# Performance work log

Measured on AMD Instinct MI355X. Metric: run time of the kernel, lower is better.

## Reference

```python
import jax, jax.numpy as jnp
import numpy as np

EPS_TRAP = 1e-8
EPS_F32 = float(np.finfo(np.float32).eps)


def _trapmf(x, a, b, c, d):
    # All args broadcastable; returns trapezoidal membership in [0,1].
    rise = (x - a) / (b - a + EPS_TRAP)
    fall = (d - x) / (d - c + EPS_TRAP)
    y = jnp.zeros_like(x + a)
    y = jnp.where((a < x) & (x < b), rise, y)
    y = jnp.where((b <= x) & (x <= c), 1.0, y)
    y = jnp.where((c < x) & (x < d), fall, y)
    return y


def setup_inputs() -> dict:
    key = jax.random.key(0)
    k1, k2, k3 = jax.random.split(key, 3)
    batch, in_dim, out_dim, n_rules = 4096, 64, 64, 256
    lo, hi = -1.0, 2.0
    x = jax.random.uniform(k1, (batch, in_dim), jnp.float32, lo, hi)
    # sorted per last-dim to satisfy a<=b<=c<=d (BreakpointIncreasingOrderConstraint)
    Antes = jnp.sort(jax.random.uniform(k2, (n_rules, in_dim, 4), jnp.float32, lo, hi), axis=-1)
    Cons = jnp.sort(jax.random.uniform(k3, (n_rules, out_dim, 4), jnp.float32, lo, hi), axis=-1)
    return {"x": x, "Antes": Antes, "Cons": Cons}


def reference(x, Antes, Cons):
    # x: (batch, in_dim); Antes: (n_rules, in_dim, 4); Cons: (n_rules, out_dim, 4)
    a = Antes[:, None, :, 0]  # (n_rules, 1, in_dim)
    b = Antes[:, None, :, 1]
    c = Antes[:, None, :, 2]
    d = Antes[:, None, :, 3]
    memb = _trapmf(x[None, :, :], a, b, c, d)      # (n_rules, batch, in_dim)
    w = jnp.min(memb, axis=-1).T                   # (batch, n_rules)
    w = w[:, :, None]                              # (batch, n_rules, 1)

    A = Cons[None, :, :, 0]  # (1, n_rules, out_dim)
    B = Cons[None, :, :, 1]
    C = Cons[None, :, :, 2]
    D = Cons[None, :, :, 3]

    term1 = 3.0 * w * (D**2 - A**2) * (1.0 - w)
    term2 = 3.0 * w**2 * (C * D - A * B)
    term3 = w**3 * (C - D + A - B) * (C - D - A + B)
    num = term1 + term2 + term3                    # (batch, n_rules, out_dim)
    den = 2.0 * w * (D - A) + w**2 * (C + A - D - B) + EPS_F32

    num_sum = num.sum(axis=1)                      # (batch, out_dim)
    den_sum = den.sum(axis=1)
    Ys = jnp.where(den_sum != 0, num_sum / den_sum, 0.0)
    return Ys / 3.0
```

## Files before the change

kernel.cpp:

```cpp
#include <hip/hip_runtime.h>


#define EPS_TRAP 1e-8f
#define EPS_F32  1.1920928955078125e-07f

constexpr int BATCH   = 4096;
constexpr int IN_DIM  = 64;
constexpr int OUT_DIM = 64;
constexpr int N_RULES = 256;

__global__ __launch_bounds__(256) void w_kernel(
    const float*  __restrict__ x,
    const float4* __restrict__ Antes,
    float* __restrict__ W,
    unsigned* __restrict__ flags)
{
    __shared__ float xs[IN_DIM][65];

    int tid  = threadIdx.x;
    int nblk = blockIdx.x & 63;
    int rgrp = blockIdx.x >> 6;
    int n0   = nblk * 64;

    #pragma unroll
    for (int k = 0; k < 4; ++k) {
        int flat = tid + k * 256;
        int nl = flat >> 4;
        int i4 = (flat & 15) * 4;
        float4 v = *reinterpret_cast<const float4*>(x + (n0 + nl) * IN_DIM + i4);
        xs[i4 + 0][nl] = v.x;
        xs[i4 + 1][nl] = v.y;
        xs[i4 + 2][nl] = v.z;
        xs[i4 + 3][nl] = v.w;
    }
    __syncthreads();

    int lane = tid & 63;
    int wvu  = __builtin_amdgcn_readfirstlane(tid >> 6);
    int r0   = rgrp * 64 + wvu * 16;

    unsigned mask = 0;
    for (int g = 0; g < 4; ++g) {
        int rb4 = r0 + g * 4;
        const float4* __restrict__ ap = Antes + rb4 * IN_DIM;

        float m[4] = {1e30f, 1e30f, 1e30f, 1e30f};
        for (int ib = 0; ib < IN_DIM; ib += 8) {
            #pragma unroll
            for (int io = 0; io < 8; ++io) {
                int i = ib + io;
                float xv = xs[i][lane];
                #pragma unroll
                for (int rr = 0; rr < 4; ++rr) {
                    float4 q = ap[rr * IN_DIM + i];
                    m[rr] = fminf(m[rr], fminf(xv - q.x, q.w - xv));
                }
            }
            float mx = fmaxf(fmaxf(m[0], m[1]), fmaxf(m[2], m[3]));
            if (!__any(mx > 0.0f)) break;
        }

        unsigned gf = 0;
        #pragma unroll
        for (int rr = 0; rr < 4; ++rr)
            if (__any(m[rr] > 0.0f)) gf |= 1u << rr;

        if (gf) {
            for (int rr = 0; rr < 4; ++rr) {
                if (!(gf & (1u << rr))) continue;
                const float4* __restrict__ aq = ap + rr * IN_DIM;
                float wm = 1e30f;
                for (int i = 0; i < IN_DIM; ++i) {
                    float4 q = aq[i];
                    float iba = 1.0f / (q.y - q.x + EPS_TRAP);
                    float idc = 1.0f / (q.w - q.z + EPS_TRAP);
                    float xv = xs[i][lane];
                    wm = fminf(wm, fminf((xv - q.x) * iba, (q.w - xv) * idc));
                }
                float w = fminf(fmaxf(wm, 0.0f), 1.0f);
                W[(rb4 + rr) * BATCH + n0 + lane] = w;
            }
        }
        mask |= gf << (g * 4);
    }
    if (lane == 0) flags[nblk * 16 + rgrp * 4 + wvu] = mask;
}

__global__ __launch_bounds__(256) void combine_kernel(
    const float*  __restrict__ W,
    const float4* __restrict__ Cons,
    const unsigned* __restrict__ flags,
    float* __restrict__ out)
{
    __shared__ unsigned fw[16];
    __shared__ float lN[4][16][64];
    __shared__ float lD[4][16][64];

    int tid   = threadIdx.x;
    int nbase = blockIdx.x * 16;
    int nblk  = blockIdx.x >> 2;

    if (tid < 16) fw[tid] = flags[nblk * 16 + tid];
    __syncthreads();

    unsigned any = 0;
    #pragma unroll
    for (int i = 0; i < 16; ++i) any |= fw[i];

    if (any == 0u) {
        reinterpret_cast<float4*>(out)[blockIdx.x * 256 + tid] =
            make_float4(0.f, 0.f, 0.f, 0.f);
        return;
    }

    int lane = tid & 63;
    int wv   = __builtin_amdgcn_readfirstlane(tid >> 6);

    unsigned long long mask =
        (unsigned long long)fw[wv * 4 + 0]        |
        ((unsigned long long)fw[wv * 4 + 1] << 16) |
        ((unsigned long long)fw[wv * 4 + 2] << 32) |
        ((unsigned long long)fw[wv * 4 + 3] << 48);
    int rbase = wv * 64;

    float num[16], den[16];
    #pragma unroll
    for (int k = 0; k < 16; ++k) { num[k] = 0.0f; den[k] = 0.0f; }

    while (mask) {
        int lr = __ffsll(mask) - 1;
        mask &= mask - 1;
        int r = rbase + lr;

        float4 c = Cons[r * OUT_DIM + lane];
        float A = c.x, B = c.y, C = c.z, D = c.w;
        float c1 = 3.0f * (D * D - A * A);
        float c2 = 3.0f * (C * D - A * B) - c1;
        float c3 = (C - D + A - B) * (C - D - A + B);
        float d1 = 2.0f * (D - A);
        float d2 = C + A - D - B;

        const float* __restrict__ wp = W + r * BATCH + nbase;
        #pragma unroll
        for (int k = 0; k < 16; ++k) {
            float w = wp[k];
            float tn = fmaf(fmaf(c3, w, c2), w, c1);
            num[k] = fmaf(tn, w, num[k]);
            den[k] = fmaf(fmaf(d2, w, d1), w, den[k]);
        }
    }

    #pragma unroll
    for (int k = 0; k < 16; ++k) { lN[wv][k][lane] = num[k]; lD[wv][k][lane] = den[k]; }
    __syncthreads();

    #pragma unroll
    for (int kk = 0; kk < 4; ++kk) {
        int row = (tid >> 6) * 4 + kk;
        float n = lN[0][row][lane] + lN[1][row][lane] +
                  lN[2][row][lane] + lN[3][row][lane];
        float d = lD[0][row][lane] + lD[1][row][lane] +
                  lD[2][row][lane] + lD[3][row][lane];
        d += (float)N_RULES * EPS_F32;
        out[(nbase + row) * OUT_DIM + lane] = (d != 0.0f) ? (n / d) * (1.0f / 3.0f) : 0.0f;
    }
}

__global__ __launch_bounds__(256) void fused_kernel(
    const float*  __restrict__ x,
    const float4* __restrict__ Antes,
    const float4* __restrict__ Cons,
    float* __restrict__ out)
{
    __shared__ float xs[IN_DIM][9];
    __shared__ float wl[N_RULES][9];

    int n0 = blockIdx.x * 8;
    int t  = threadIdx.x;

    for (int k = 0; k < 2; ++k) {
        int idx = t * 2 + k;
        int nl = idx >> 6, i = idx & 63;
        xs[i][nl] = x[(n0 + nl) * IN_DIM + i];
    }
    __syncthreads();

    {
        float wmin[8];
        #pragma unroll
        for (int n = 0; n < 8; ++n) wmin[n] = 1e30f;
        const float4* ap = Antes + t * IN_DIM;
        for (int i = 0; i < IN_DIM; ++i) {
            float4 q = ap[i];
            float iba = 1.0f / (q.y - q.x + EPS_TRAP);
            float idc = 1.0f / (q.w - q.z + EPS_TRAP);
            float na = -q.x * iba, dq = q.w * idc;
            #pragma unroll
            for (int n = 0; n < 8; ++n) {
                float xv = xs[i][n];
                float y = fminf(fmaf(xv, iba, na), fmaf(xv, -idc, dq));
                y = fminf(fmaxf(y, 0.0f), 1.0f);
                wmin[n] = fminf(wmin[n], y);
            }
        }
        #pragma unroll
        for (int n = 0; n < 8; ++n) wl[t][n] = wmin[n];
    }
    __syncthreads();

    int lane = t & 63, wv = t >> 6;
    float num0 = 0.f, den0 = 0.f, num1 = 0.f, den1 = 0.f;
    for (int r = 0; r < N_RULES; ++r) {
        float4 c = Cons[r * OUT_DIM + lane];
        float A = c.x, B = c.y, C = c.z, D = c.w;
        float c1 = 3.0f * (D * D - A * A);
        float c2 = 3.0f * (C * D - A * B) - c1;
        float c3 = (C - D + A - B) * (C - D - A + B);
        float d1 = 2.0f * (D - A);
        float d2 = C + A - D - B;
        float wa = wl[r][wv * 2], wb = wl[r][wv * 2 + 1];
        float wa2 = wa * wa, wa3 = wa2 * wa;
        float wb2 = wb * wb, wb3 = wb2 * wb;
        num0 = fmaf(c1, wa, num0); num0 = fmaf(c2, wa2, num0); num0 = fmaf(c3, wa3, num0);
        den0 = fmaf(d1, wa, den0); den0 = fmaf(d2, wa2, den0);
        num1 = fmaf(c1, wb, num1); num1 = fmaf(c2, wb2, num1); num1 = fmaf(c3, wb3, num1);
        den1 = fmaf(d1, wb, den1); den1 = fmaf(d2, wb2, den1);
    }
    den0 += 256.0f * EPS_F32;
    den1 += 256.0f * EPS_F32;
    float y0 = (den0 != 0.0f) ? num0 / den0 : 0.0f;
    float y1 = (den1 != 0.0f) ? num1 / den1 : 0.0f;
    out[(n0 + wv * 2) * OUT_DIM + lane]     = y0 * (1.0f / 3.0f);
    out[(n0 + wv * 2 + 1) * OUT_DIM + lane] = y1 * (1.0f / 3.0f);
}

extern "C" void kernel_launch(void* const* d_in, const int* in_sizes, int n_in,
                              void* d_out, int out_size, void* d_ws, size_t ws_size,
                              hipStream_t stream) {
    const float* x     = (const float*)d_in[0];
    const float* Antes = (const float*)d_in[1];
    const float* Cons  = (const float*)d_in[2];
    float* out = (float*)d_out;

    const size_t W_BYTES  = (size_t)N_RULES * BATCH * 4;
    const size_t FL_BYTES = 64 * 16 * sizeof(unsigned);
    const size_t NEED = W_BYTES + FL_BYTES;

    if (ws_size >= NEED) {
        char* p = (char*)d_ws;
        float*    Wp    = (float*)p;      p += W_BYTES;
        unsigned* flags = (unsigned*)p;

        w_kernel<<<256, 256, 0, stream>>>(x, (const float4*)Antes, Wp, flags);
        combine_kernel<<<256, 256, 0, stream>>>(Wp, (const float4*)Cons, flags, out);
    } else {
        fused_kernel<<<512, 256, 0, stream>>>(x, (const float4*)Antes,
                                              (const float4*)Cons, out);
    }
}
```

Before: 14.90 us.

## Fuse membership and combine kernels into one block-per-64-rows kernel using LDS

Merges the two-kernel pipeline (a firing-strength kernel writing W and flags to global workspace, then a combine kernel) into one kernel with 1024-thread blocks. Each block handles 64 batch rows, keeps the rule weights and active-rule flags in shared memory, and then accumulates the consequent terms over only the active rules. This removes the second launch and the global round trip of the W matrix. In exchange the grid shrinks to 64 large blocks, which leaves many CUs idle, and the per-block work on the Antes scan grows.

```diff
diff --git a/kernel.cpp b/kernel.cpp
--- a/kernel.cpp
+++ b/kernel.cpp
@@ -9,24 +9,22 @@
 constexpr int OUT_DIM = 64;
 constexpr int N_RULES = 256;
 
-__global__ __launch_bounds__(256) void w_kernel(
+__global__ __launch_bounds__(1024) void fuzzy_fused_kernel(
     const float*  __restrict__ x,
     const float4* __restrict__ Antes,
-    float* __restrict__ W,
-    unsigned* __restrict__ flags)
+    const float4* __restrict__ Cons,
+    float* __restrict__ out)
 {
-    __shared__ float xs[IN_DIM][65];
+    __shared__ float    xs[IN_DIM][65];
+    __shared__ float    Wlds[N_RULES][64];
+    __shared__ unsigned fl[16];
 
-    int tid  = threadIdx.x;
-    int nblk = blockIdx.x & 63;
-    int rgrp = blockIdx.x >> 6;
-    int n0   = nblk * 64;
+    int tid = threadIdx.x;
+    int n0  = blockIdx.x * 64;
 
-    #pragma unroll
-    for (int k = 0; k < 4; ++k) {
-        int flat = tid + k * 256;
-        int nl = flat >> 4;
-        int i4 = (flat & 15) * 4;
+    {
+        int nl = tid >> 4;
+        int i4 = (tid & 15) * 4;
         float4 v = *reinterpret_cast<const float4*>(x + (n0 + nl) * IN_DIM + i4);
         xs[i4 + 0][nl] = v.x;
         xs[i4 + 1][nl] = v.y;
@@ -37,9 +35,9 @@
 
     int lane = tid & 63;
     int wvu  = __builtin_amdgcn_readfirstlane(tid >> 6);
-    int r0   = rgrp * 64 + wvu * 16;
+    int r0   = wvu * 16;
 
-    unsigned mask = 0;
+    unsigned bits = 0;
     for (int g = 0; g < 4; ++g) {
         int rb4 = r0 + g * 4;
         const float4* __restrict__ ap = Antes + rb4 * IN_DIM;
@@ -77,161 +75,66 @@
                     float xv = xs[i][lane];
                     wm = fminf(wm, fminf((xv - q.x) * iba, (q.w - xv) * idc));
                 }
-                float w = fminf(fmaxf(wm, 0.0f), 1.0f);
-                W[(rb4 + rr) * BATCH + n0 + lane] = w;
+                Wlds[rb4 + rr][lane] = fminf(fmaxf(wm, 0.0f), 1.0f);
             }
         }
-        mask |= gf << (g * 4);
+        bits |= gf << (g * 4);
     }
-    if (lane == 0) flags[nblk * 16 + rgrp * 4 + wvu] = mask;
-}
-
-__global__ __launch_bounds__(256) void combine_kernel(
-    const float*  __restrict__ W,
-    const float4* __restrict__ Cons,
-    const unsigned* __restrict__ flags,
-    float* __restrict__ out)
-{
-    __shared__ unsigned fw[16];
-    __shared__ float lN[4][16][64];
-    __shared__ float lD[4][16][64];
-
-    int tid   = threadIdx.x;
-    int nbase = blockIdx.x * 16;
-    int nblk  = blockIdx.x >> 2;
-
-    if (tid < 16) fw[tid] = flags[nblk * 16 + tid];
+    if (lane == 0) fl[wvu] = bits;
     __syncthreads();
 
     unsigned any = 0;
     #pragma unroll
-    for (int i = 0; i < 16; ++i) any |= fw[i];
+    for (int i = 0; i < 16; ++i) any |= fl[i];
 
     if (any == 0u) {
-        reinterpret_cast<float4*>(out)[blockIdx.x * 256 + tid] =
+        reinterpret_cast<float4*>(out)[blockIdx.x * 1024 + tid] =
             make_float4(0.f, 0.f, 0.f, 0.f);
         return;
     }
 
-    int lane = tid & 63;
-    int wv   = __builtin_amdgcn_readfirstlane(tid >> 6);
+    float num[4] = {0.f, 0.f, 0.f, 0.f};
+    float den[4] = {0.f, 0.f, 0.f, 0.f};
+    int row0 = wvu * 4;
 
-    unsigned long long mask =
-        (unsigned long long)fw[wv * 4 + 0]        |
-        ((unsigned long long)fw[wv * 4 + 1] << 16) |
-        ((unsigned long long)fw[wv * 4 + 2] << 32) |
-        ((unsigned long long)fw[wv * 4 + 3] << 48);
-    int rbase = wv * 64;
+    #pragma unroll
+    for (int w4 = 0; w4 < 4; ++w4) {
+        unsigned long long mask =
+            (unsigned long long)__builtin_amdgcn_readfirstlane(fl[w4 * 4 + 0])        |
+            ((unsigned long long)__builtin_amdgcn_readfirstlane(fl[w4 * 4 + 1]) << 16) |
+            ((unsigned long long)__builtin_amdgcn_readfirstlane(fl[w4 * 4 + 2]) << 32) |
+            ((unsigned long long)__builtin_amdgcn_readfirstlane(fl[w4 * 4 + 3]) << 48);
+        int rbase = w4 * 64;
 
-    float num[16], den[16];
-    #pragma unroll
-    for (int k = 0; k < 16; ++k) { num[k] = 0.0f; den[k] = 0.0f; }
+        while (mask) {
+            int lr = __ffsll(mask) - 1;
+            mask &= mask - 1;
+            int r = rbase + lr;
 
-    while (mask) {
-        int lr = __ffsll(mask) - 1;
-        mask &= mask - 1;
-        int r = rbase + lr;
+            float4 c = Cons[r * OUT_DIM + lane];
+            float A = c.x, B = c.y, C = c.z, D = c.w;
+            float c1 = 3.0f * (D * D - A * A);
+            float c2 = 3.0f * (C * D - A * B) - c1;
+            float c3 = (C - D + A - B) * (C - D - A + B);
+            float d1 = 2.0f * (D - A);
+            float d2 = C + A - D - B;
 
-        float4 c = Cons[r * OUT_DIM + lane];
-        float A = c.x, B = c.y, C = c.z, D = c.w;
-        float c1 = 3.0f * (D * D - A * A);
-        float c2 = 3.0f * (C * D - A * B) - c1;
-        float c3 = (C - D + A - B) * (C - D - A + B);
-        float d1 = 2.0f * (D - A);
-        float d2 = C + A - D - B;
-
-        const float* __restrict__ wp = W + r * BATCH + nbase;
-        #pragma unroll
-        for (int k = 0; k < 16; ++k) {
-            float w = wp[k];
-            float tn = fmaf(fmaf(c3, w, c2), w, c1);
-            num[k] = fmaf(tn, w, num[k]);
-            den[k] = fmaf(fmaf(d2, w, d1), w, den[k]);
+            #pragma unroll
+            for (int k = 0; k < 4; ++k) {
+                float w = Wlds[r][row0 + k];
+                float tn = fmaf(fmaf(c3, w, c2), w, c1);
+                num[k] = fmaf(tn, w, num[k]);
+                den[k] = fmaf(fmaf(d2, w, d1), w, den[k]);
+            }
         }
     }
 
     #pragma unroll
-    for (int k = 0; k < 16; ++k) { lN[wv][k][lane] = num[k]; lD[wv][k][lane] = den[k]; }
-    __syncthreads();
-
-    #pragma unroll
-    for (int kk = 0; kk < 4; ++kk) {
-        int row = (tid >> 6) * 4 + kk;
-        float n = lN[0][row][lane] + lN[1][row][lane] +
-                  lN[2][row][lane] + lN[3][row][lane];
-        float d = lD[0][row][lane] + lD[1][row][lane] +
-                  lD[2][row][lane] + lD[3][row][lane];
-        d += (float)N_RULES * EPS_F32;
-        out[(nbase + row) * OUT_DIM + lane] = (d != 0.0f) ? (n / d) * (1.0f / 3.0f) : 0.0f;
+    for (int k = 0; k < 4; ++k) {
+        float d = den[k] + (float)N_RULES * EPS_F32;
+        out[(n0 + row0 + k) * OUT_DIM + lane] =
+            (d != 0.0f) ? (num[k] / d) * (1.0f / 3.0f) : 0.0f;
     }
-}
-
-__global__ __launch_bounds__(256) void fused_kernel(
-    const float*  __restrict__ x,
-    const float4* __restrict__ Antes,
-    const float4* __restrict__ Cons,
-    float* __restrict__ out)
-{
-    __shared__ float xs[IN_DIM][9];
-    __shared__ float wl[N_RULES][9];
-
-    int n0 = blockIdx.x * 8;
-    int t  = threadIdx.x;
-
-    for (int k = 0; k < 2; ++k) {
-        int idx = t * 2 + k;
-        int nl = idx >> 6, i = idx & 63;
-        xs[i][nl] = x[(n0 + nl) * IN_DIM + i];
-    }
-    __syncthreads();
-
-    {
-        float wmin[8];
-        #pragma unroll
-        for (int n = 0; n < 8; ++n) wmin[n] = 1e30f;
-        const float4* ap = Antes + t * IN_DIM;
-        for (int i = 0; i < IN_DIM; ++i) {
-            float4 q = ap[i];
-            float iba = 1.0f / (q.y - q.x + EPS_TRAP);
-            float idc = 1.0f / (q.w - q.z + EPS_TRAP);
-            float na = -q.x * iba, dq = q.w * idc;
-            #pragma unroll
-            for (int n = 0; n < 8; ++n) {
-                float xv = xs[i][n];
-                float y = fminf(fmaf(xv, iba, na), fmaf(xv, -idc, dq));
-                y = fminf(fmaxf(y, 0.0f), 1.0f);
-                wmin[n] = fminf(wmin[n], y);
-            }
-        }
-        #pragma unroll
-        for (int n = 0; n < 8; ++n) wl[t][n] = wmin[n];
-    }
-    __syncthreads();
-
-    int lane = t & 63, wv = t >> 6;
-    float num0 = 0.f, den0 = 0.f, num1 = 0.f, den1 = 0.f;
-    for (int r = 0; r < N_RULES; ++r) {
-        float4 c = Cons[r * OUT_DIM + lane];
-        float A = c.x, B = c.y, C = c.z, D = c.w;
-        float c1 = 3.0f * (D * D - A * A);
-        float c2 = 3.0f * (C * D - A * B) - c1;
-        float c3 = (C - D + A - B) * (C - D - A + B);
-        float d1 = 2.0f * (D - A);
-        float d2 = C + A - D - B;
-        float wa = wl[r][wv * 2], wb = wl[r][wv * 2 + 1];
-        float wa2 = wa * wa, wa3 = wa2 * wa;
-        float wb2 = wb * wb, wb3 = wb2 * wb;
-        num0 = fmaf(c1, wa, num0); num0 = fmaf(c2, wa2, num0); num0 = fmaf(c3, wa3, num0);
-        den0 = fmaf(d1, wa, den0); den0 = fmaf(d2, wa2, den0);
-        num1 = fmaf(c1, wb, num1); num1 = fmaf(c2, wb2, num1); num1 = fmaf(c3, wb3, num1);
-        den1 = fmaf(d1, wb, den1); den1 = fmaf(d2, wb2, den1);
-    }
-    den0 += 256.0f * EPS_F32;
-    den1 += 256.0f * EPS_F32;
-    float y0 = (den0 != 0.0f) ? num0 / den0 : 0.0f;
-    float y1 = (den1 != 0.0f) ? num1 / den1 : 0.0f;
-    out[(n0 + wv * 2) * OUT_DIM + lane]     = y0 * (1.0f / 3.0f);
-    out[(n0 + wv * 2 + 1) * OUT_DIM + lane] = y1 * (1.0f / 3.0f);
 }
 
 extern "C" void kernel_launch(void* const* d_in, const int* in_sizes, int n_in,
@@ -242,19 +145,6 @@
     const float* Cons  = (const float*)d_in[2];
     float* out = (float*)d_out;
 
-    const size_t W_BYTES  = (size_t)N_RULES * BATCH * 4;
-    const size_t FL_BYTES = 64 * 16 * sizeof(unsigned);
-    const size_t NEED = W_BYTES + FL_BYTES;
-
-    if (ws_size >= NEED) {
-        char* p = (char*)d_ws;
-        float*    Wp    = (float*)p;      p += W_BYTES;
-        unsigned* flags = (unsigned*)p;
-
-        w_kernel<<<256, 256, 0, stream>>>(x, (const float4*)Antes, Wp, flags);
-        combine_kernel<<<256, 256, 0, stream>>>(Wp, (const float4*)Cons, flags, out);
-    } else {
-        fused_kernel<<<512, 256, 0, stream>>>(x, (const float4*)Antes,
-                                              (const float4*)Cons, out);
-    }
+    fuzzy_fused_kernel<<<64, 1024, 0, stream>>>(
+        x, (const float4*)Antes, (const float4*)Cons, out);
 }
```

Result: slower. 16.80 us (+12.7%).
